# Kernel tuning notes

Hardware: AMD Instinct MI355X
Metric: run time of the kernel (lower is better)

## Reference

```python
import jax, jax.numpy as jnp
import numpy as np

D_MODEL, D_KEY, D_VALUE, H = 1024, 64, 64, 16
B, S = 4, 2048

def setup_inputs() -> dict:
    key = jax.random.key(0)
    ks = jax.random.split(key, 11)
    sd = 1.0 / np.sqrt(D_MODEL)
    return {
        "queries": jax.random.normal(ks[0], (B, S, D_MODEL), jnp.float32),
        "keys": jax.random.normal(ks[1], (B, S, D_MODEL), jnp.float32),
        "values": jax.random.normal(ks[2], (B, S, D_MODEL), jnp.float32),
        "Wq": jax.random.normal(ks[3], (D_MODEL, H * D_KEY), jnp.float32) * sd,
        "bq": jax.random.normal(ks[4], (H * D_KEY,), jnp.float32) * 0.01,
        "Wk": jax.random.normal(ks[5], (D_MODEL, H * D_KEY), jnp.float32) * sd,
        "bk": jax.random.normal(ks[6], (H * D_KEY,), jnp.float32) * 0.01,
        "Wv": jax.random.normal(ks[7], (D_MODEL, H * D_VALUE), jnp.float32) * sd,
        "bv": jax.random.normal(ks[8], (H * D_VALUE,), jnp.float32) * 0.01,
        "Wo": jax.random.normal(ks[9], (H * D_VALUE, D_MODEL), jnp.float32) * sd,
        "bo": jax.random.normal(ks[10], (D_MODEL,), jnp.float32) * 0.01,
    }

def reference(queries, keys, values, Wq, bq, Wk, bk, Wv, bv, Wo, bo):
    bs, nq, _ = queries.shape
    nk = keys.shape[1]
    # projections -> [b, h, s, d]
    q = (queries @ Wq + bq).reshape(bs, nq, H, D_KEY).transpose(0, 2, 1, 3)
    k = (keys @ Wk + bk).reshape(bs, nk, H, D_KEY).transpose(0, 2, 1, 3)
    v = (values @ Wv + bv).reshape(bs, nk, H, D_VALUE).transpose(0, 2, 1, 3)
    att = jnp.einsum('bhqd,bhkd->bhqk', q, k) / np.sqrt(D_KEY).astype(np.float32)
    att = jax.nn.softmax(att, axis=-1)  # dropout is identity in eval mode
    out = jnp.einsum('bhqk,bhkd->bhqd', att, v)
    out = out.transpose(0, 2, 1, 3).reshape(bs, nq, H * D_VALUE)
    return out @ Wo + bo
```

## Files before the change

kernel.cpp:

```cpp
#include <hip/hip_runtime.h>
#include <hip/hip_bf16.h>
#include <stdint.h>

#define DM 1024
#define DKH 64
#define NH 16
#define NB 4
#define SEQ 2048

typedef __attribute__((ext_vector_type(8))) short bf16x8;
typedef __attribute__((ext_vector_type(4))) short bf16x4;
typedef __attribute__((ext_vector_type(8))) unsigned short ushort8;
typedef __attribute__((ext_vector_type(4))) float f32x4;

union S8 { bf16x8 w; bf16x4 h[2]; };

__device__ inline unsigned short f2bf(float f) {
  union { float f; unsigned u; } c; c.f = f;
  unsigned u = c.u;
  u += 0x7fff + ((u >> 16) & 1);
  return (unsigned short)(u >> 16);
}

#define GLOAD16(dst, ptr, OFF)                                              \
  asm volatile("global_load_dwordx4 %0, %1, off offset:" #OFF               \
               : "=v"(dst) : "v"(ptr))

#define WAITV(N)                                            \
  do {                                                      \
    asm volatile("s_waitcnt vmcnt(" #N ")" ::: "memory");   \
    __builtin_amdgcn_sched_barrier(0);                      \
  } while (0)

__device__ inline void glds16(const unsigned short* g, unsigned short* l) {
  __builtin_amdgcn_global_load_lds(
      (const __attribute__((address_space(1))) unsigned int*)g,
      (__attribute__((address_space(3))) unsigned int*)l, 16, 0, 0);
}

__device__ inline void mfma16x16x16(f32x4& acc, bf16x4 a, bf16x4 b) {
  asm("v_mfma_f32_16x16x16_bf16 %0, %1, %2, %0" : "+v"(acc) : "v"(a), "v"(b));
}

__global__ __launch_bounds__(256) void acast(const float* __restrict__ A,
                                             unsigned short* __restrict__ O) {
  size_t i = ((size_t)blockIdx.x * 256 + threadIdx.x) * 8;
  const float* p = A + i;
  float4 x = *reinterpret_cast<const float4*>(p);
  float4 y = *reinterpret_cast<const float4*>(p + 4);
  ushort8 v;
  v[0] = f2bf(x.x); v[1] = f2bf(x.y); v[2] = f2bf(x.z); v[3] = f2bf(x.w);
  v[4] = f2bf(y.x); v[5] = f2bf(y.y); v[6] = f2bf(y.z); v[7] = f2bf(y.w);
  *reinterpret_cast<ushort8*>(O + i) = v;
}

__global__ __launch_bounds__(256) void wcast_all(const float* __restrict__ W0,
                                                 const float* __restrict__ W1,
                                                 const float* __restrict__ W2,
                                                 const float* __restrict__ W3,
                                                 unsigned short* __restrict__ Wt0,
                                                 unsigned short* __restrict__ Wt1,
                                                 unsigned short* __restrict__ Wt2,
                                                 unsigned short* __restrict__ Wt3) {
  __shared__ float tile[32][33];
  int z = blockIdx.z;
  const float* W = z == 0 ? W0 : z == 1 ? W1 : z == 2 ? W2 : W3;
  unsigned short* Wt = z == 0 ? Wt0 : z == 1 ? Wt1 : z == 2 ? Wt2 : Wt3;
  int bk = blockIdx.x * 32, bn = blockIdx.y * 32;
  int tx = threadIdx.x & 31, ty = threadIdx.x >> 5;
#pragma unroll
  for (int i = 0; i < 4; ++i)
    tile[ty + 8 * i][tx] = W[(size_t)(bk + ty + 8 * i) * DM + bn + tx];
  __syncthreads();
#pragma unroll
  for (int i = 0; i < 4; ++i)
    Wt[(size_t)(bn + ty + 8 * i) * DM + bk + tx] = f2bf(tile[tx][ty + 8 * i]);
}

template <int EPI>
__global__ __launch_bounds__(256) void gemm_bf16(const unsigned short* __restrict__ A,
                                                 const unsigned short* __restrict__ Bt,
                                                 const float* __restrict__ bias,
                                                 void* __restrict__ Cv, float scale) {
  __shared__ __align__(16) unsigned short As[2][128][32];
  __shared__ __align__(16) unsigned short Bs[2][128][32];
  const int K = DM;
  int t = threadIdx.x;
  int wave = t >> 6, lane = t & 63;
  int wr = wave >> 1, wc = wave & 1;
  int l15 = lane & 15, g = lane >> 4;
  int bid = blockIdx.x;
  int xcd = bid & 7, ii = bid >> 3;
  int tn = ii >> 3;
  int tm = ((ii & 7) << 3) | xcd;
  int rowBase = tm * 128, colBase = tn * 128;

  f32x4 acc[4][4];
#pragma unroll
  for (int mi = 0; mi < 4; ++mi)
#pragma unroll
    for (int ni = 0; ni < 4; ++ni) acc[mi][ni] = (f32x4){0.f, 0.f, 0.f, 0.f};

  const unsigned short* sa0 =
      A + (size_t)(rowBase + wave * 16 + (lane >> 2)) * K + (lane & 3) * 8;
  const unsigned short* sa1 = sa0 + (size_t)64 * K;
  const unsigned short* sb0 =
      Bt + (size_t)(colBase + wave * 16 + (lane >> 2)) * K + (lane & 3) * 8;
  const unsigned short* sb1 = sb0 + (size_t)64 * K;

#define STAGE(BUF)                                   \
  do {                                               \
    glds16(sa0, &As[BUF][wave * 16][0]);             \
    glds16(sa1, &As[BUF][64 + wave * 16][0]);        \
    glds16(sb0, &Bs[BUF][wave * 16][0]);             \
    glds16(sb1, &Bs[BUF][64 + wave * 16][0]);        \
    sa0 += 32; sa1 += 32; sb0 += 32; sb1 += 32;      \
  } while (0)

#define COMPUTE(BUF)                                                            \
  do {                                                                          \
    bf16x8 af[4], bfr[4];                                                       \
    _Pragma("unroll")                                                           \
    for (int mi = 0; mi < 4; ++mi)                                              \
      af[mi] = *reinterpret_cast<const bf16x8*>(                                \
          &As[BUF][wr * 64 + mi * 16 + l15][g * 8]);                            \
    _Pragma("unroll")                                                           \
    for (int ni = 0; ni < 4; ++ni)                                              \
      bfr[ni] = *reinterpret_cast<const bf16x8*>(                               \
          &Bs[BUF][wc * 64 + ni * 16 + l15][g * 8]);                            \
    _Pragma("unroll")                                                           \
    for (int mi = 0; mi < 4; ++mi)                                              \
      _Pragma("unroll")                                                         \
      for (int ni = 0; ni < 4; ++ni)                                            \
        acc[mi][ni] = __builtin_amdgcn_mfma_f32_16x16x32_bf16(af[mi], bfr[ni],  \
                                                              acc[mi][ni], 0, 0, 0); \
  } while (0)

  STAGE(0);
#pragma unroll 1
  for (int it = 0; it < 16; ++it) {
    __syncthreads();
    STAGE(1);
    WAITV(4);
    __syncthreads();
    COMPUTE(0);
    __syncthreads();
    if (it < 15) {
      STAGE(0);
      WAITV(4);
    } else {
      WAITV(0);
    }
    __syncthreads();
    COMPUTE(1);
  }
#undef STAGE
#undef COMPUTE

#pragma unroll
  for (int ni = 0; ni < 4; ++ni) {
    int col = colBase + wc * 64 + ni * 16 + l15;
    float bvv = bias[col];
#pragma unroll
    for (int mi = 0; mi < 4; ++mi) {
#pragma unroll
      for (int r = 0; r < 4; ++r) {
        int row = rowBase + wr * 64 + mi * 16 + g * 4 + r;
        float val = (acc[mi][ni][r] + bvv) * scale;
        if (EPI == 3) {
          ((float*)Cv)[(size_t)row * DM + col] = val;
        } else {
          int b_ = row >> 11, s_ = row & 2047;
          int h_ = col >> 6, d_ = col & 63;
          size_t hb = (size_t)(b_ * NH + h_) * (SEQ * DKH);
          size_t idx;
          if (EPI == 0) {
            idx = hb + (size_t)s_ * DKH + d_;
          } else if (EPI == 1) {
            idx = hb + (size_t)(s_ >> 4) * 1024 + (d_ >> 5) * 512 +
                  ((d_ >> 3) & 3) * 128 + (s_ & 15) * 8 + (d_ & 7);
          } else {
            idx = hb + (size_t)(s_ >> 5) * 2048 + (d_ >> 4) * 512 +
                  ((s_ >> 2) & 3) * 128 + (d_ & 15) * 8 + ((s_ >> 4) & 1) * 4 +
                  (s_ & 3);
          }
          ((unsigned short*)Cv)[idx] = f2bf(val);
        }
      }
    }
  }
}

__global__ __launch_bounds__(256) void attn_fwd(const unsigned short* __restrict__ Qb,
                                                const unsigned short* __restrict__ Kp_,
                                                const unsigned short* __restrict__ Vp_,
                                                unsigned short* __restrict__ AO) {
  int t = threadIdx.x;
  int wave = t >> 6, lane = t & 63;
  int l15 = lane & 15, g = lane >> 4;
  int bid = blockIdx.x;
  int xcd = bid & 7, j = bid >> 3;
  int bh = (xcd << 3) | (j >> 4);
  int qtile = j & 15;
  const size_t baseH = (size_t)bh * SEQ * DKH;
  int q0 = qtile * 128 + wave * 32;

  bf16x8 aQ[2][2];
#pragma unroll
  for (int qf = 0; qf < 2; ++qf)
#pragma unroll
    for (int dh = 0; dh < 2; ++dh)
      aQ[qf][dh] = *reinterpret_cast<const bf16x8*>(
          Qb + baseH + (size_t)(q0 + qf * 16 + l15) * DKH + dh * 32 + g * 8);

  float lsum[2] = {0.f, 0.f};
  f32x4 accO[2][4];
#pragma unroll
  for (int qf = 0; qf < 2; ++qf)
#pragma unroll
    for (int dt = 0; dt < 4; ++dt) accO[qf][dt] = (f32x4){0.f, 0.f, 0.f, 0.f};

  int ck = wave * 16;
  const unsigned short* kp = Kp_ + baseH + (size_t)ck * 2048 + g * 128 + l15 * 8;
  const unsigned short* vp = Vp_ + baseH + (size_t)ck * 2048 + (size_t)lane * 8;

  bf16x8 k0[2][2], k1[2][2], k2[2][2];
  S8 v0[4], v1[4], v2[4];
  bf16x4 pf[2][2];

#define ISSUE_KV(kbuf, vbuf)                          \
  do {                                                \
    GLOAD16(kbuf[0][0], kp, 0);                       \
    GLOAD16(kbuf[0][1], kp, 1024);                    \
    GLOAD16(kbuf[1][0], kp, 2048);                    \
    GLOAD16(kbuf[1][1], kp, 3072);                    \
    GLOAD16(vbuf[0].w, vp, 0);                        \
    GLOAD16(vbuf[1].w, vp, 1024);                     \
    GLOAD16(vbuf[2].w, vp, 2048);                     \
    GLOAD16(vbuf[3].w, vp, 3072);                     \
    kp += 2048; vp += 2048;                           \
    if (++ck == 64) {                                 \
      ck = 0;                                         \
      kp -= (size_t)SEQ * DKH;                        \
      vp -= (size_t)SEQ * DKH;                        \
    }                                                 \
  } while (0)

  const f32x4 ZOFF = (f32x4){-16.f, -16.f, -16.f, -16.f};

  auto qksm = [&](const bf16x8 (&kf)[2][2]) {
    f32x4 sc[2][2];
    __builtin_amdgcn_s_setprio(1);
#pragma unroll
    for (int qf = 0; qf < 2; ++qf)
#pragma unroll
      for (int tt = 0; tt < 2; ++tt) {
        f32x4 z = ZOFF;
#pragma unroll
        for (int dh = 0; dh < 2; ++dh)
          z = __builtin_amdgcn_mfma_f32_16x16x32_bf16(kf[tt][dh], aQ[qf][dh], z, 0, 0, 0);
        sc[qf][tt] = z;
      }
    __builtin_amdgcn_s_setprio(0);
#pragma unroll
    for (int qf = 0; qf < 2; ++qf) {
      float pv[8];
#pragma unroll
      for (int tt = 0; tt < 2; ++tt)
#pragma unroll
        for (int r = 0; r < 4; ++r)
          pv[tt * 4 + r] = __builtin_amdgcn_exp2f(sc[qf][tt][r]);
      lsum[qf] +=
          ((pv[0] + pv[1]) + (pv[2] + pv[3])) + ((pv[4] + pv[5]) + (pv[6] + pv[7]));
#pragma unroll
      for (int tt = 0; tt < 2; ++tt) {
        unsigned w0, w1;
        asm("v_cvt_pk_bf16_f32 %0, %1, %2"
            : "=v"(w0) : "v"(pv[tt * 4 + 0]), "v"(pv[tt * 4 + 1]));
        asm("v_cvt_pk_bf16_f32 %0, %1, %2"
            : "=v"(w1) : "v"(pv[tt * 4 + 2]), "v"(pv[tt * 4 + 3]));
        union { unsigned u[2]; bf16x4 v; } pk;
        pk.u[0] = w0; pk.u[1] = w1;
        pf[qf][tt] = pk.v;
      }
    }
  };

  auto pvstep = [&](const S8 (&vf)[4]) {
    __builtin_amdgcn_s_setprio(1);
#pragma unroll
    for (int qf = 0; qf < 2; ++qf)
#pragma unroll
      for (int tt = 0; tt < 2; ++tt)
#pragma unroll
        for (int dt = 0; dt < 4; ++dt)
          mfma16x16x16(accO[qf][dt], vf[dt].h[tt], pf[qf][tt]);
    __builtin_amdgcn_s_setprio(0);
  };

  ISSUE_KV(k0, v0);
  ISSUE_KV(k1, v1);
  ISSUE_KV(k2, v2);

  for (int it = 0; it < 21; ++it) {
    WAITV(20); qksm(k0); WAITV(16); pvstep(v0); ISSUE_KV(k0, v0);
    WAITV(20); qksm(k1); WAITV(16); pvstep(v1); ISSUE_KV(k1, v1);
    WAITV(20); qksm(k2); WAITV(16); pvstep(v2); ISSUE_KV(k2, v2);
  }
  WAITV(20); qksm(k0); WAITV(16); pvstep(v0);
  WAITV(0);
#undef ISSUE_KV

  int b_ = bh >> 4, h_ = bh & 15;
#pragma unroll
  for (int qf = 0; qf < 2; ++qf) {
    float ls = lsum[qf];
    ls += __shfl_xor(ls, 16);
    ls += __shfl_xor(ls, 32);
    float inv = 1.f / ls;
    int sq = q0 + qf * 16 + l15;
#pragma unroll
    for (int dt = 0; dt < 4; ++dt)
#pragma unroll
      for (int r = 0; r < 4; ++r) {
        float val = accO[qf][dt][r] * inv;
        AO[(size_t)(b_ * SEQ + sq) * DM + h_ * DKH + dt * 16 + g * 4 + r] = f2bf(val);
      }
  }
}

extern "C" void kernel_launch(void* const* d_in, const int* in_sizes, int n_in,
                              void* d_out, int out_size, void* d_ws, size_t ws_size,
                              hipStream_t stream) {
  (void)in_sizes; (void)n_in; (void)out_size; (void)ws_size;
  const float* queries = (const float*)d_in[0];
  const float* keys = (const float*)d_in[1];
  const float* values = (const float*)d_in[2];
  const float* Wq = (const float*)d_in[3];
  const float* bq = (const float*)d_in[4];
  const float* Wk = (const float*)d_in[5];
  const float* bk = (const float*)d_in[6];
  const float* Wv = (const float*)d_in[7];
  const float* bv = (const float*)d_in[8];
  const float* Wo = (const float*)d_in[9];
  const float* bo = (const float*)d_in[10];
  float* out = (float*)d_out;

  char* ws = (char*)d_ws;
  unsigned short* wt_q = (unsigned short*)(ws + 0 * (1u << 21));
  unsigned short* wt_k = (unsigned short*)(ws + 1 * (1u << 21));
  unsigned short* wt_v = (unsigned short*)(ws + 2 * (1u << 21));
  unsigned short* wt_o = (unsigned short*)(ws + 3 * (1u << 21));
  unsigned short* Qb = (unsigned short*)(ws + (8u << 20));
  unsigned short* Kb = (unsigned short*)(ws + (24u << 20));
  unsigned short* Vt = (unsigned short*)(ws + (40u << 20));
  unsigned short* AO = (unsigned short*)(ws + (56u << 20));

  const float SQ = 0.125f * 1.4426950408889634f;

  wcast_all<<<dim3(32, 32, 4), 256, 0, stream>>>(Wq, Wk, Wv, Wo,
                                                 wt_q, wt_k, wt_v, wt_o);
  acast<<<4096, 256, 0, stream>>>(queries, AO);
  gemm_bf16<0><<<512, 256, 0, stream>>>(AO, wt_q, bq, Qb, SQ);
  acast<<<4096, 256, 0, stream>>>(keys, AO);
  gemm_bf16<1><<<512, 256, 0, stream>>>(AO, wt_k, bk, Kb, 1.0f);
  acast<<<4096, 256, 0, stream>>>(values, AO);
  gemm_bf16<2><<<512, 256, 0, stream>>>(AO, wt_v, bv, Vt, 1.0f);
  attn_fwd<<<1024, 256, 0, stream>>>(Qb, Kb, Vt, AO);
  gemm_bf16<3><<<512, 256, 0, stream>>>(AO, wt_o, bo, out, 1.0f);
}
```

Baseline: 238.2 us.

## Software-pipeline QK and PV across iterations with double-buffered probabilities

Restructures the attention inner loop so each step issues the QK MFMAs for the current key chunk together with the PV MFMAs for the previous chunk's probabilities, then computes softmax exp. The probabilities are double-buffered in pfA/pfB. This lets the exp/convert work overlap with matrix ops and reduces waits. It also drops the per-wave rotated key start offset and its wraparound check, so all waves walk the key chunks in the same order. That may raise cache contention but removes branch logic. The added buffers raise register pressure.

Result: faster. 233.2 us (-2.1%).

```diff
diff --git a/kernel.cpp b/kernel.cpp
--- a/kernel.cpp
+++ b/kernel.cpp
@@ -220,13 +220,12 @@
 #pragma unroll
     for (int dt = 0; dt < 4; ++dt) accO[qf][dt] = (f32x4){0.f, 0.f, 0.f, 0.f};
 
-  int ck = wave * 16;
-  const unsigned short* kp = Kp_ + baseH + (size_t)ck * 2048 + g * 128 + l15 * 8;
-  const unsigned short* vp = Vp_ + baseH + (size_t)ck * 2048 + (size_t)lane * 8;
+  const unsigned short* kp = Kp_ + baseH + g * 128 + l15 * 8;
+  const unsigned short* vp = Vp_ + baseH + (size_t)lane * 8;
 
   bf16x8 k0[2][2], k1[2][2], k2[2][2];
   S8 v0[4], v1[4], v2[4];
-  bf16x4 pf[2][2];
+  bf16x4 pfA[2][2], pfB[2][2];
 
 #define ISSUE_KV(kbuf, vbuf)                          \
   do {                                                \
@@ -239,18 +238,11 @@
     GLOAD16(vbuf[2].w, vp, 2048);                     \
     GLOAD16(vbuf[3].w, vp, 3072);                     \
     kp += 2048; vp += 2048;                           \
-    if (++ck == 64) {                                 \
-      ck = 0;                                         \
-      kp -= (size_t)SEQ * DKH;                        \
-      vp -= (size_t)SEQ * DKH;                        \
-    }                                                 \
   } while (0)
 
   const f32x4 ZOFF = (f32x4){-16.f, -16.f, -16.f, -16.f};
 
-  auto qksm = [&](const bf16x8 (&kf)[2][2]) {
-    f32x4 sc[2][2];
-    __builtin_amdgcn_s_setprio(1);
+  auto qk = [&](const bf16x8 (&kf)[2][2], f32x4 (&sc)[2][2]) {
 #pragma unroll
     for (int qf = 0; qf < 2; ++qf)
 #pragma unroll
@@ -261,24 +253,26 @@
           z = __builtin_amdgcn_mfma_f32_16x16x32_bf16(kf[tt][dh], aQ[qf][dh], z, 0, 0, 0);
         sc[qf][tt] = z;
       }
-    __builtin_amdgcn_s_setprio(0);
+  };
+
+  auto smx = [&](const f32x4 (&sc)[2][2], bf16x4 (&pf)[2][2]) {
 #pragma unroll
     for (int qf = 0; qf < 2; ++qf) {
-      float pv[8];
+      float pv_[8];
 #pragma unroll
       for (int tt = 0; tt < 2; ++tt)
 #pragma unroll
         for (int r = 0; r < 4; ++r)
-          pv[tt * 4 + r] = __builtin_amdgcn_exp2f(sc[qf][tt][r]);
+          pv_[tt * 4 + r] = __builtin_amdgcn_exp2f(sc[qf][tt][r]);
       lsum[qf] +=
-          ((pv[0] + pv[1]) + (pv[2] + pv[3])) + ((pv[4] + pv[5]) + (pv[6] + pv[7]));
+          ((pv_[0] + pv_[1]) + (pv_[2] + pv_[3])) + ((pv_[4] + pv_[5]) + (pv_[6] + pv_[7]));
 #pragma unroll
       for (int tt = 0; tt < 2; ++tt) {
         unsigned w0, w1;
         asm("v_cvt_pk_bf16_f32 %0, %1, %2"
-            : "=v"(w0) : "v"(pv[tt * 4 + 0]), "v"(pv[tt * 4 + 1]));
+            : "=v"(w0) : "v"(pv_[tt * 4 + 0]), "v"(pv_[tt * 4 + 1]));
         asm("v_cvt_pk_bf16_f32 %0, %1, %2"
-            : "=v"(w1) : "v"(pv[tt * 4 + 2]), "v"(pv[tt * 4 + 3]));
+            : "=v"(w1) : "v"(pv_[tt * 4 + 2]), "v"(pv_[tt * 4 + 3]));
         union { unsigned u[2]; bf16x4 v; } pk;
         pk.u[0] = w0; pk.u[1] = w1;
         pf[qf][tt] = pk.v;
@@ -286,8 +280,7 @@
     }
   };
 
-  auto pvstep = [&](const S8 (&vf)[4]) {
-    __builtin_amdgcn_s_setprio(1);
+  auto pv = [&](const S8 (&vf)[4], const bf16x4 (&pf)[2][2]) {
 #pragma unroll
     for (int qf = 0; qf < 2; ++qf)
 #pragma unroll
@@ -295,20 +288,61 @@
 #pragma unroll
         for (int dt = 0; dt < 4; ++dt)
           mfma16x16x16(accO[qf][dt], vf[dt].h[tt], pf[qf][tt]);
-    __builtin_amdgcn_s_setprio(0);
   };
+
+#define BODY(KQ, VP, PIN, POUT, KI, VI)               \
+  do {                                                \
+    WAITV(8);                                         \
+    f32x4 sc[2][2];                                   \
+    __builtin_amdgcn_s_setprio(1);                    \
+    qk(KQ, sc);                                       \
+    pv(VP, PIN);                                      \
+    __builtin_amdgcn_s_setprio(0);                    \
+    smx(sc, POUT);                                    \
+    ISSUE_KV(KI, VI);                                 \
+  } while (0)
 
   ISSUE_KV(k0, v0);
   ISSUE_KV(k1, v1);
-  ISSUE_KV(k2, v2);
-
-  for (int it = 0; it < 21; ++it) {
-    WAITV(20); qksm(k0); WAITV(16); pvstep(v0); ISSUE_KV(k0, v0);
-    WAITV(20); qksm(k1); WAITV(16); pvstep(v1); ISSUE_KV(k1, v1);
-    WAITV(20); qksm(k2); WAITV(16); pvstep(v2); ISSUE_KV(k2, v2);
-  }
-  WAITV(20); qksm(k0); WAITV(16); pvstep(v0);
-  WAITV(0);
+  {
+    WAITV(8);
+    f32x4 sc[2][2];
+    __builtin_amdgcn_s_setprio(1);
+    qk(k0, sc);
+    __builtin_amdgcn_s_setprio(0);
+    smx(sc, pfA);
+    ISSUE_KV(k2, v2);
+  }
+#pragma unroll 1
+  for (int it = 0; it < 10; ++it) {
+    BODY(k1, v0, pfA, pfB, k0, v0);
+    BODY(k2, v1, pfB, pfA, k1, v1);
+    BODY(k0, v2, pfA, pfB, k2, v2);
+    BODY(k1, v0, pfB, pfA, k0, v0);
+    BODY(k2, v1, pfA, pfB, k1, v1);
+    BODY(k0, v2, pfB, pfA, k2, v2);
+  }
+  BODY(k1, v0, pfA, pfB, k0, v0);
+  {
+    WAITV(8);
+    f32x4 sc[2][2];
+    __builtin_amdgcn_s_setprio(1);
+    qk(k2, sc);
+    pv(v1, pfB);
+    __builtin_amdgcn_s_setprio(0);
+    smx(sc, pfA);
+  }
+  {
+    WAITV(0);
+    f32x4 sc[2][2];
+    __builtin_amdgcn_s_setprio(1);
+    qk(k0, sc);
+    pv(v2, pfA);
+    __builtin_amdgcn_s_setprio(0);
+    smx(sc, pfB);
+  }
+  pv(v0, pfB);
+#undef BODY
 #undef ISSUE_KV
 
   int b_ = bh >> 4, h_ = bh & 15;
```
